# Performance work log

Hardware: AMD Instinct MI355X
Metric: run time of the kernel (lower is better)

## Reference

```python
import jax, jax.numpy as jnp
import numpy as np

N_NODES = 100000
N_EDGES = 1600000
IN_RAW = 64
HID = 128


def setup_inputs() -> dict:
    key = jax.random.key(0)
    ks = jax.random.split(key, 16)
    inp = {
        "x": jax.random.normal(ks[0], (N_NODES, IN_RAW), dtype=jnp.float32),
        "edge_index": jax.random.randint(ks[1], (2, N_EDGES), 0, N_NODES, dtype=jnp.int64),
        "user_ids": jax.random.randint(ks[2], (N_NODES,), 0, 10000, dtype=jnp.int64),
        "locations": jax.random.randint(ks[3], (N_NODES,), 0, 1000, dtype=jnp.int64),
        "time_features": jax.random.normal(ks[4], (N_NODES, 4), dtype=jnp.float32),
        # embeddings / encoders
        "user_emb_table": jax.random.normal(ks[5], (10000, 32), dtype=jnp.float32) * 0.02,
        "loc_emb_table": jax.random.normal(ks[6], (1000, 16), dtype=jnp.float32) * 0.02,
        "W_time": jax.random.normal(ks[7], (4, 16), dtype=jnp.float32) * 0.1,
        "b_time": jnp.zeros((16,), dtype=jnp.float32),
        # SAGEConv 1: lin_l (aggregated, with bias), lin_r (root, no bias)
        "W1_l": jax.random.normal(ks[8], (HID, HID), dtype=jnp.float32) * (1.0 / np.sqrt(HID)),
        "b1": jnp.zeros((HID,), dtype=jnp.float32),
        "W1_r": jax.random.normal(ks[9], (HID, HID), dtype=jnp.float32) * (1.0 / np.sqrt(HID)),
        # SAGEConv 2
        "W2_l": jax.random.normal(ks[10], (HID, HID), dtype=jnp.float32) * (1.0 / np.sqrt(HID)),
        "b2": jnp.zeros((HID,), dtype=jnp.float32),
        "W2_r": jax.random.normal(ks[11], (HID, HID), dtype=jnp.float32) * (1.0 / np.sqrt(HID)),
        # classifier
        "Wc": jax.random.normal(ks[12], (HID, 1), dtype=jnp.float32) * (1.0 / np.sqrt(HID)),
        "bc": jnp.zeros((1,), dtype=jnp.float32),
    }
    return inp


def _sage_conv(h, src, dst, W_l, b_l, W_r, n_nodes):
    # mean aggregation of source features onto targets (PyG SAGEConv default)
    msg_sum = jax.ops.segment_sum(h[src], dst, num_segments=n_nodes)  # [N, D]
    deg = jax.ops.segment_sum(jnp.ones((src.shape[0],), h.dtype), dst, num_segments=n_nodes)
    agg = msg_sum / jnp.maximum(deg, 1.0)[:, None]
    return agg @ W_l + b_l + h @ W_r


def reference(x, edge_index, user_ids, locations, time_features,
              user_emb_table, loc_emb_table, W_time, b_time,
              W1_l, b1, W1_r, W2_l, b2, W2_r, Wc, bc):
    n = x.shape[0]
    src, dst = edge_index[0], edge_index[1]
    user_emb = user_emb_table[user_ids]            # [N, 32]
    loc_emb = loc_emb_table[locations]             # [N, 16]
    time_emb = time_features @ W_time + b_time     # [N, 16]
    h = jnp.concatenate([x, user_emb, loc_emb, time_emb], axis=-1)  # [N, 128]
    h = jax.nn.relu(_sage_conv(h, src, dst, W1_l, b1, W1_r, n))  # dropout = identity (eval)
    h = jax.nn.relu(_sage_conv(h, src, dst, W2_l, b2, W2_r, n))
    return jax.nn.sigmoid(h @ Wc + bc)  # [N, 1]
```

## Files before the change

### kernel.cpp

```cpp
#include <hip/hip_runtime.h>
#include <math.h>

#define N_NODES 100000
#define HID 128
#define NB 782
#define CAP 4096
#define NBLK 256
#define BTILE 6250
#define SUBCAP 32
#define SCAP 3072
#define WPB 64

typedef __attribute__((ext_vector_type(8))) short bf16x8;
typedef __attribute__((ext_vector_type(4))) float f32x4;
typedef __attribute__((ext_vector_type(2))) float f32x2;

__device__ __forceinline__ unsigned short f2bf(float f) {
  union { float f; unsigned u; } v; v.f = f;
  unsigned r = v.u + 0x7FFFu + ((v.u >> 16) & 1u);
  return (unsigned short)(r >> 16);
}
__device__ __forceinline__ unsigned packbf(float lo, float hi) {
  return (unsigned)f2bf(lo) | ((unsigned)f2bf(hi) << 16);
}
__device__ __forceinline__ unsigned pkfp8x4(float a, float b, float c, float d) {
  int v = __builtin_amdgcn_cvt_pk_fp8_f32(a, b, 0, false);
  v = __builtin_amdgcn_cvt_pk_fp8_f32(c, d, v, true);
  return (unsigned)v;
}
__device__ __forceinline__ float bflo(unsigned u) {
  union { unsigned u; float f; } v; v.u = u << 16; return v.f;
}
__device__ __forceinline__ float bfhi(unsigned u) {
  union { unsigned u; float f; } v; v.u = u & 0xFFFF0000u; return v.f;
}
__device__ __forceinline__ void acc_add_fp8(float* a, unsigned w) {
  f32x2 p0 = __builtin_amdgcn_cvt_pk_f32_fp8((int)w, false);
  f32x2 p1 = __builtin_amdgcn_cvt_pk_f32_fp8((int)w, true);
  a[0] += p0.x; a[1] += p0.y; a[2] += p1.x; a[3] += p1.y;
}
__device__ __forceinline__ void acc_add_row(float* a, uint4 u) {
  acc_add_fp8(a + 0, u.x);
  acc_add_fp8(a + 4, u.y);
  acc_add_fp8(a + 8, u.z);
  acc_add_fp8(a + 12, u.w);
}

__global__ __launch_bounds__(256) void k_embed(
    const float* __restrict__ x, const int* __restrict__ uid,
    const int* __restrict__ lid, const float* __restrict__ timef,
    const float* __restrict__ utab, const float* __restrict__ ltab,
    const float* __restrict__ Wt, const float* __restrict__ bt,
    unsigned short* __restrict__ h0, unsigned char* __restrict__ h0f8) {
  int t = threadIdx.x;
  int v = blockIdx.x * 16 + (t >> 4);
  int g = t & 15;
  if (v >= N_NODES) return;
  float val[8];
  if (g < 8) {
    const float4* xp = (const float4*)&x[(size_t)v * 64 + g * 8];
    float4 a = xp[0], b = xp[1];
    val[0] = a.x; val[1] = a.y; val[2] = a.z; val[3] = a.w;
    val[4] = b.x; val[5] = b.y; val[6] = b.z; val[7] = b.w;
  } else if (g < 12) {
    const float4* up = (const float4*)&utab[(size_t)uid[v] * 32 + (g - 8) * 8];
    float4 a = up[0], b = up[1];
    val[0] = a.x; val[1] = a.y; val[2] = a.z; val[3] = a.w;
    val[4] = b.x; val[5] = b.y; val[6] = b.z; val[7] = b.w;
  } else if (g < 14) {
    const float4* lp = (const float4*)&ltab[(size_t)lid[v] * 16 + (g - 12) * 8];
    float4 a = lp[0], b = lp[1];
    val[0] = a.x; val[1] = a.y; val[2] = a.z; val[3] = a.w;
    val[4] = b.x; val[5] = b.y; val[6] = b.z; val[7] = b.w;
  } else {
    int c0 = (g - 14) * 8;
    float4 tf = *(const float4*)&timef[(size_t)v * 4];
#pragma unroll
    for (int i = 0; i < 8; ++i) {
      int c = c0 + i;
      val[i] = bt[c] + tf.x * Wt[c] + tf.y * Wt[16 + c] + tf.z * Wt[32 + c] +
               tf.w * Wt[48 + c];
    }
  }
  uint4 ob;
  ob.x = packbf(val[0], val[1]);
  ob.y = packbf(val[2], val[3]);
  ob.z = packbf(val[4], val[5]);
  ob.w = packbf(val[6], val[7]);
  *(uint4*)&h0[(size_t)v * 128 + g * 8] = ob;
  uint2 of;
  of.x = pkfp8x4(val[0], val[1], val[2], val[3]);
  of.y = pkfp8x4(val[4], val[5], val[6], val[7]);
  *(uint2*)&h0f8[(size_t)v * 128 + g * 8] = of;
}

__global__ __launch_bounds__(512) void k_bucket(
    const int* __restrict__ src, const int* __restrict__ dst,
    int* __restrict__ gcnt, unsigned* __restrict__ bdata2, int E) {
  __shared__ int hcnt[NB];
  int t = threadIdx.x;
  int blk = blockIdx.x;
  int e0 = blk * BTILE;
  int e1 = min(e0 + BTILE, E);
  for (int i = t; i < NB; i += 512) hcnt[i] = 0;
  __syncthreads();
#pragma unroll 4
  for (int e = e0 + t; e < e1; e += 512) {
    int d = dst[e], s = src[e];
    int b = d >> 7;
    int pos = atomicAdd(&hcnt[b], 1);
    if (pos < SUBCAP)
      bdata2[((size_t)blk * NB + b) * SUBCAP + pos] =
          ((unsigned)s << 7) | (unsigned)(d & 127);
  }
  __syncthreads();
  for (int i = t; i < NB; i += 512)
    gcnt[blk * NB + i] = hcnt[i];
}

__global__ __launch_bounds__(256) void k_bfill(
    const int* __restrict__ gcnt, const unsigned* __restrict__ bdata2,
    int* __restrict__ rstart, int* __restrict__ rdeg, int* __restrict__ col,
    const float* __restrict__ W1l, const float* __restrict__ W1r,
    const float* __restrict__ W2l, const float* __restrict__ W2r,
    unsigned short* __restrict__ WT) {
  int b = blockIdx.x;
  int t = threadIdx.x;
  if (b >= NB) {
    int lin = ((b - NB) * 256 + t) * 4;
    int m = lin >> 14;
    int rem = lin & 16383;
    int f = rem >> 7;
    int k0 = rem & 127;
    const float* W = (m == 0) ? W1l : (m == 1) ? W1r : (m == 2) ? W2l : W2r;
    unsigned short o[4];
#pragma unroll
    for (int j = 0; j < 4; ++j) o[j] = f2bf(W[(size_t)(k0 + j) * 128 + f]);
    uint2 pk;
    pk.x = (unsigned)o[0] | ((unsigned)o[1] << 16);
    pk.y = (unsigned)o[2] | ((unsigned)o[3] << 16);
    *(uint2*)&WT[m * 16384 + f * 128 + k0] = pk;
    return;
  }
  __shared__ unsigned sdata[SCAP];
  __shared__ int soff[NBLK];
  __shared__ int scnt[NBLK];
  __shared__ int wsum[4];
  __shared__ int lcnt[128];
  __shared__ int wtot;
  int lane = t & 63, wv = t >> 6;

  int c = (t < NBLK) ? min(gcnt[t * NB + b], SUBCAP) : 0;
  int x = c;
#pragma unroll
  for (int off = 1; off < 64; off <<= 1) {
    int v = __shfl_up(x, off);
    if (lane >= off) x += v;
  }
  if (lane == 63) wsum[wv] = x;
  __syncthreads();
  int add = 0;
#pragma unroll
  for (int k = 0; k < 4; ++k)
    if (k < wv) add += wsum[k];
  x += add;
  int tot = min(wsum[0] + wsum[1] + wsum[2] + wsum[3], SCAP);
  if (t < NBLK) { soff[t] = x - c; scnt[t] = c; }
  if (t < 128) lcnt[t] = 0;
  __syncthreads();

  for (int i = t; i < NBLK * 8; i += 256) {
    int j = i >> 3, p4 = (i & 7) * 4;
    int cj = scnt[j];
    if (p4 < cj) {
      uint4 v = *(const uint4*)&bdata2[((size_t)j * NB + b) * SUBCAP + p4];
      int bs = soff[j] + p4;
      int n = min(4, cj - p4);
      unsigned vv[4] = {v.x, v.y, v.z, v.w};
#pragma unroll
      for (int e = 0; e < 4; ++e)
        if (e < n && bs + e < SCAP) sdata[bs + e] = vv[e];
    }
  }
  __syncthreads();

  for (int i = t; i < tot; i += 256) atomicAdd(&lcnt[sdata[i] & 127u], 1);
  __syncthreads();

  int node0 = b * 128;
  int base = b * CAP;
  if (t < 128) {
    int cc = lcnt[t];
    int xx = cc;
#pragma unroll
    for (int off = 1; off < 64; off <<= 1) {
      int v = __shfl_up(xx, off);
      if (lane >= off) xx += v;
    }
    if (t == 63) wtot = xx;
    __syncthreads();
    if (t >= 64) xx += wtot;
    int excl = xx - cc;
    if (node0 + t < N_NODES) {
      rstart[node0 + t] = base + excl;
      rdeg[node0 + t] = cc;
    }
    lcnt[t] = excl;
  } else {
    __syncthreads();
  }
  __syncthreads();
  for (int i = t; i < tot; i += 256) {
    unsigned v = sdata[i];
    int pos = base + atomicAdd(&lcnt[v & 127u], 1);
    col[pos] = (int)(v >> 7);
  }
}

__global__ __launch_bounds__(256) void k_agg(
    const unsigned char* __restrict__ hf8, const int* __restrict__ rstart,
    const int* __restrict__ rdeg, const int* __restrict__ col,
    unsigned short* __restrict__ agg) {
  int t = threadIdx.x;
  int v = blockIdx.x * 32 + (t >> 3);
  int q = t & 7;
  if (v >= N_NODES) return;
  int s0 = rstart[v];
  int deg = rdeg[v];
  int s1 = s0 + deg;
  const uint4* h8 = (const uint4*)hf8;
  float acc[16];
#pragma unroll
  for (int i = 0; i < 16; ++i) acc[i] = 0.f;
  int j = s0;
  for (; j + 4 <= s1; j += 4) {
    uint4 r0 = h8[(size_t)col[j] * 8 + q];
    uint4 r1 = h8[(size_t)col[j + 1] * 8 + q];
    uint4 r2 = h8[(size_t)col[j + 2] * 8 + q];
    uint4 r3 = h8[(size_t)col[j + 3] * 8 + q];
    acc_add_row(acc, r0);
    acc_add_row(acc, r1);
    acc_add_row(acc, r2);
    acc_add_row(acc, r3);
  }
  for (; j < s1; ++j) acc_add_row(acc, h8[(size_t)col[j] * 8 + q]);
  float inv = 1.f / (float)(deg > 0 ? deg : 1);
  uint4 o0, o1;
  o0.x = packbf(acc[0] * inv, acc[1] * inv);
  o0.y = packbf(acc[2] * inv, acc[3] * inv);
  o0.z = packbf(acc[4] * inv, acc[5] * inv);
  o0.w = packbf(acc[6] * inv, acc[7] * inv);
  o1.x = packbf(acc[8] * inv, acc[9] * inv);
  o1.y = packbf(acc[10] * inv, acc[11] * inv);
  o1.z = packbf(acc[12] * inv, acc[13] * inv);
  o1.w = packbf(acc[14] * inv, acc[15] * inv);
  ((uint4*)agg)[(size_t)v * 16 + q * 2] = o0;
  ((uint4*)agg)[(size_t)v * 16 + q * 2 + 1] = o1;
}

template <bool CLS>
__global__ __launch_bounds__(256, 4) void k_gemm(
    const unsigned short* __restrict__ agg, const unsigned short* __restrict__ hin,
    const unsigned short* __restrict__ WlT, const unsigned short* __restrict__ WrT,
    const float* __restrict__ bias, unsigned short* __restrict__ hout,
    unsigned char* __restrict__ houtf8,
    const float* __restrict__ Wc, const float* __restrict__ bc,
    float* __restrict__ out) {
  __shared__ unsigned short SB[2 * 64 * 136];
  unsigned short* As = SB;
  unsigned short* Hs = SB + 64 * 136;
  unsigned short* Ot = SB;
  float* zred = (float*)SB;
  int t = threadIdx.x;
  int lane = t & 63;
  int wave = t >> 6;
  int wn = wave * 32;
  int l15 = lane & 15;
  int quad = lane >> 4;
  int mbase = blockIdx.x * 64;

  {
    int r = t >> 2, seg = t & 3;
    int gn = mbase + r;
    uint4 av[4], hv[4];
    if (gn < N_NODES) {
      const uint4* ap = (const uint4*)(agg + (size_t)gn * 128 + seg * 32);
      const uint4* hp = (const uint4*)(hin + (size_t)gn * 128 + seg * 32);
#pragma unroll
      for (int i = 0; i < 4; ++i) { av[i] = ap[i]; hv[i] = hp[i]; }
    } else {
#pragma unroll
      for (int i = 0; i < 4; ++i) { av[i] = make_uint4(0,0,0,0); hv[i] = make_uint4(0,0,0,0); }
    }
#pragma unroll
    for (int i = 0; i < 4; ++i) {
      *(uint4*)&As[r * 136 + seg * 32 + i * 8] = av[i];
      *(uint4*)&Hs[r * 136 + seg * 32 + i * 8] = hv[i];
    }
  }
  __syncthreads();

  f32x4 acc4[4][2];
#pragma unroll
  for (int i = 0; i < 4; ++i)
#pragma unroll
    for (int j = 0; j < 2; ++j) acc4[i][j] = (f32x4){0.f, 0.f, 0.f, 0.f};

#pragma unroll
  for (int ks = 0; ks < 4; ++ks) {
    int kb = ks * 32 + quad * 8;
    bf16x8 bL[2], bR[2];
#pragma unroll
    for (int jn = 0; jn < 2; ++jn) {
      int f = wn + jn * 16 + l15;
      bL[jn] = *(const bf16x8*)&WlT[(size_t)f * 128 + kb];
      bR[jn] = *(const bf16x8*)&WrT[(size_t)f * 128 + kb];
    }
    bf16x8 aA[4], aH[4];
#pragma unroll
    for (int im = 0; im < 4; ++im) {
      aA[im] = *(const bf16x8*)&As[(im * 16 + l15) * 136 + kb];
      aH[im] = *(const bf16x8*)&Hs[(im * 16 + l15) * 136 + kb];
    }
#pragma unroll
    for (int im = 0; im < 4; ++im)
#pragma unroll
      for (int jn = 0; jn < 2; ++jn)
        acc4[im][jn] = __builtin_amdgcn_mfma_f32_16x16x32_bf16(
            aA[im], bL[jn], acc4[im][jn], 0, 0, 0);
#pragma unroll
    for (int im = 0; im < 4; ++im)
#pragma unroll
      for (int jn = 0; jn < 2; ++jn)
        acc4[im][jn] = __builtin_amdgcn_mfma_f32_16x16x32_bf16(
            aH[im], bR[jn], acc4[im][jn], 0, 0, 0);
  }

  float bv[2];
#pragma unroll
  for (int jn = 0; jn < 2; ++jn) bv[jn] = bias[wn + jn * 16 + l15];

  __syncthreads();

  if (!CLS) {
#pragma unroll
    for (int im = 0; im < 4; ++im)
#pragma unroll
      for (int rr = 0; rr < 4; ++rr) {
        int rloc = im * 16 + quad * 4 + rr;
#pragma unroll
        for (int jn = 0; jn < 2; ++jn)
          Ot[rloc * 136 + wn + jn * 16 + l15] =
              f2bf(fmaxf(acc4[im][jn][rr] + bv[jn], 0.f));
      }
    __syncthreads();
    int r = t >> 2, seg = t & 3;
    int node = mbase + r;
    if (node < N_NODES) {
      uint4 d0[4];
      const uint4* srcp = (const uint4*)&Ot[r * 136 + seg * 32];
      uint4* dstp = (uint4*)&hout[(size_t)node * 128 + seg * 32];
#pragma unroll
      for (int i = 0; i < 4; ++i) { d0[i] = srcp[i]; dstp[i] = d0[i]; }
      unsigned w[8];
#pragma unroll
      for (int i = 0; i < 4; ++i) {
        unsigned u[4] = {d0[i].x, d0[i].y, d0[i].z, d0[i].w};
#pragma unroll
        for (int p = 0; p < 2; ++p) {
          w[i * 2 + p] = pkfp8x4(bflo(u[p * 2]), bfhi(u[p * 2]),
                                 bflo(u[p * 2 + 1]), bfhi(u[p * 2 + 1]));
        }
      }
      uint4* fp = (uint4*)&houtf8[(size_t)node * 128 + seg * 32];
      fp[0] = make_uint4(w[0], w[1], w[2], w[3]);
      fp[1] = make_uint4(w[4], w[5], w[6], w[7]);
    }
  } else {
    float wcv[2];
#pragma unroll
    for (int jn = 0; jn < 2; ++jn) wcv[jn] = Wc[wn + jn * 16 + l15];
#pragma unroll
    for (int im = 0; im < 4; ++im) {
#pragma unroll
      for (int rr = 0; rr < 4; ++rr) {
        float p = 0.f;
#pragma unroll
        for (int jn = 0; jn < 2; ++jn)
          p += fmaxf(acc4[im][jn][rr] + bv[jn], 0.f) * wcv[jn];
        p += __shfl_xor(p, 1);
        p += __shfl_xor(p, 2);
        p += __shfl_xor(p, 4);
        p += __shfl_xor(p, 8);
        if (l15 == 0) zred[wave * 64 + im * 16 + quad * 4 + rr] = p;
      }
    }
    __syncthreads();
    if (t < 64) {
      int node = mbase + t;
      if (node < N_NODES) {
        float z = zred[t] + zred[64 + t] + zred[128 + t] + zred[192 + t] + bc[0];
        out[node] = 1.f / (1.f + expf(-z));
      }
    }
  }
}

extern "C" void kernel_launch(void* const* d_in, const int* in_sizes, int n_in,
                              void* d_out, int out_size, void* d_ws, size_t ws_size,
                              hipStream_t stream) {
  const float* x     = (const float*)d_in[0];
  const int*   eidx  = (const int*)d_in[1];
  const int*   uid   = (const int*)d_in[2];
  const int*   lid   = (const int*)d_in[3];
  const float* timef = (const float*)d_in[4];
  const float* utab  = (const float*)d_in[5];
  const float* ltab  = (const float*)d_in[6];
  const float* Wt    = (const float*)d_in[7];
  const float* bt    = (const float*)d_in[8];
  const float* W1l   = (const float*)d_in[9];
  const float* b1    = (const float*)d_in[10];
  const float* W1r   = (const float*)d_in[11];
  const float* W2l   = (const float*)d_in[12];
  const float* b2    = (const float*)d_in[13];
  const float* W2r   = (const float*)d_in[14];
  const float* Wc    = (const float*)d_in[15];
  const float* bc    = (const float*)d_in[16];
  float* out = (float*)d_out;

  const int E = in_sizes[1] / 2;
  const int* src = eidx;
  const int* dst = eidx + E;

  char* ws = (char*)d_ws;
  size_t off = 0;
  auto alloc = [&](size_t bytes) -> void* {
    void* p = ws + off;
    off += (bytes + 255) & ~(size_t)255;
    return p;
  };
  const size_t HBYTES = (size_t)N_NODES * 128 * sizeof(unsigned short);
  const size_t FBYTES = (size_t)N_NODES * 128;
  unsigned short* h0  = (unsigned short*)alloc(HBYTES);
  unsigned short* h1  = (unsigned short*)alloc(HBYTES);
  unsigned short* agg = (unsigned short*)alloc(HBYTES);
  unsigned char* h0f8 = (unsigned char*)alloc(FBYTES);
  unsigned char* h1f8 = (unsigned char*)alloc(FBYTES);
  unsigned short* WT  = (unsigned short*)alloc(4 * 16384 * sizeof(unsigned short));
  unsigned* bdata2    = (unsigned*)alloc((size_t)NBLK * NB * SUBCAP * 4);
  int* gcnt           = (int*)alloc((size_t)NBLK * NB * 4);
  int* col            = (int*)alloc((size_t)NB * CAP * 4);
  int* rstart         = (int*)alloc((size_t)N_NODES * 4);
  int* rdeg           = (int*)alloc((size_t)N_NODES * 4);
  (void)ws_size; (void)n_in; (void)out_size;

  k_bucket<<<NBLK, 512, 0, stream>>>(src, dst, gcnt, bdata2, E);
  k_embed<<<(N_NODES + 15) / 16, 256, 0, stream>>>(x, uid, lid, timef, utab, ltab, Wt, bt,
                                                   h0, h0f8);
  k_bfill<<<NB + WPB, 256, 0, stream>>>(gcnt, bdata2, rstart, rdeg, col,
                                        W1l, W1r, W2l, W2r, WT);

  k_agg<<<(N_NODES + 31) / 32, 256, 0, stream>>>(h0f8, rstart, rdeg, col, agg);
  k_gemm<false><<<(N_NODES + 63) / 64, 256, 0, stream>>>(
      agg, h0, WT, WT + 16384, b1, h1, h1f8, nullptr, nullptr, nullptr);

  k_agg<<<(N_NODES + 31) / 32, 256, 0, stream>>>(h1f8, rstart, rdeg, col, agg);
  k_gemm<true><<<(N_NODES + 63) / 64, 256, 0, stream>>>(
      agg, h1, WT + 32768, WT + 49152, b2, nullptr, nullptr, Wc, bc, out);
}
```

Before: 280.1 us.

## Fuse neighbor aggregation into the per-layer GEMM kernel, dropping agg buffer

Merges the gather-mean aggregation and the dual GEMM into one k_layer kernel. Each block aggregates its 64 nodes straight into shared memory, and the root features are read directly from global memory into MFMA operands instead of being staged in LDS. This removes a global write and re-read of the bf16 agg array and one launch per layer, and halves LDS use so occupancy can rise (launch bounds raised to 5). The cost is that the gather latency and the GEMM now share one block, with fewer nodes per block during the gather phase (64 nodes over two passes), and the uncoalesced global loads of hin inside the MFMA loop.

Result: no change. 285.3 us (+1.9%).

```diff
diff --git a/kernel.cpp b/kernel.cpp
--- a/kernel.cpp
+++ b/kernel.cpp
@@ -217,88 +217,71 @@
   }
 }
 
-__global__ __launch_bounds__(256) void k_agg(
-    const unsigned char* __restrict__ hf8, const int* __restrict__ rstart,
-    const int* __restrict__ rdeg, const int* __restrict__ col,
-    unsigned short* __restrict__ agg) {
-  int t = threadIdx.x;
-  int v = blockIdx.x * 32 + (t >> 3);
-  int q = t & 7;
-  if (v >= N_NODES) return;
-  int s0 = rstart[v];
-  int deg = rdeg[v];
-  int s1 = s0 + deg;
-  const uint4* h8 = (const uint4*)hf8;
-  float acc[16];
-#pragma unroll
-  for (int i = 0; i < 16; ++i) acc[i] = 0.f;
-  int j = s0;
-  for (; j + 4 <= s1; j += 4) {
-    uint4 r0 = h8[(size_t)col[j] * 8 + q];
-    uint4 r1 = h8[(size_t)col[j + 1] * 8 + q];
-    uint4 r2 = h8[(size_t)col[j + 2] * 8 + q];
-    uint4 r3 = h8[(size_t)col[j + 3] * 8 + q];
-    acc_add_row(acc, r0);
-    acc_add_row(acc, r1);
-    acc_add_row(acc, r2);
-    acc_add_row(acc, r3);
-  }
-  for (; j < s1; ++j) acc_add_row(acc, h8[(size_t)col[j] * 8 + q]);
-  float inv = 1.f / (float)(deg > 0 ? deg : 1);
-  uint4 o0, o1;
-  o0.x = packbf(acc[0] * inv, acc[1] * inv);
-  o0.y = packbf(acc[2] * inv, acc[3] * inv);
-  o0.z = packbf(acc[4] * inv, acc[5] * inv);
-  o0.w = packbf(acc[6] * inv, acc[7] * inv);
-  o1.x = packbf(acc[8] * inv, acc[9] * inv);
-  o1.y = packbf(acc[10] * inv, acc[11] * inv);
-  o1.z = packbf(acc[12] * inv, acc[13] * inv);
-  o1.w = packbf(acc[14] * inv, acc[15] * inv);
-  ((uint4*)agg)[(size_t)v * 16 + q * 2] = o0;
-  ((uint4*)agg)[(size_t)v * 16 + q * 2 + 1] = o1;
-}
-
 template <bool CLS>
-__global__ __launch_bounds__(256, 4) void k_gemm(
-    const unsigned short* __restrict__ agg, const unsigned short* __restrict__ hin,
+__global__ __launch_bounds__(256, 5) void k_layer(
+    const unsigned char* __restrict__ hf8, const unsigned short* __restrict__ hin,
+    const int* __restrict__ rstart, const int* __restrict__ rdeg,
+    const int* __restrict__ col,
     const unsigned short* __restrict__ WlT, const unsigned short* __restrict__ WrT,
     const float* __restrict__ bias, unsigned short* __restrict__ hout,
     unsigned char* __restrict__ houtf8,
     const float* __restrict__ Wc, const float* __restrict__ bc,
     float* __restrict__ out) {
-  __shared__ unsigned short SB[2 * 64 * 136];
-  unsigned short* As = SB;
-  unsigned short* Hs = SB + 64 * 136;
-  unsigned short* Ot = SB;
-  float* zred = (float*)SB;
+  __shared__ unsigned short As[64 * 136];
+  unsigned short* Ot = As;
+  float* zred = (float*)As;
   int t = threadIdx.x;
+  int mbase = blockIdx.x * 64;
+
+  {
+    int q = t & 7;
+    const uint4* h8 = (const uint4*)hf8;
+#pragma unroll
+    for (int pass = 0; pass < 2; ++pass) {
+      int ln = pass * 32 + (t >> 3);
+      int v = mbase + ln;
+      float acc[16];
+#pragma unroll
+      for (int i = 0; i < 16; ++i) acc[i] = 0.f;
+      int deg = 0;
+      if (v < N_NODES) {
+        int s0 = rstart[v];
+        deg = rdeg[v];
+        int s1 = s0 + deg;
+        int j = s0;
+        for (; j + 4 <= s1; j += 4) {
+          uint4 r0 = h8[(size_t)col[j] * 8 + q];
+          uint4 r1 = h8[(size_t)col[j + 1] * 8 + q];
+          uint4 r2 = h8[(size_t)col[j + 2] * 8 + q];
+          uint4 r3 = h8[(size_t)col[j + 3] * 8 + q];
+          acc_add_row(acc, r0);
+          acc_add_row(acc, r1);
+          acc_add_row(acc, r2);
+          acc_add_row(acc, r3);
+        }
+        for (; j < s1; ++j) acc_add_row(acc, h8[(size_t)col[j] * 8 + q]);
+      }
+      float inv = 1.f / (float)(deg > 0 ? deg : 1);
+      uint4 o0, o1;
+      o0.x = packbf(acc[0] * inv, acc[1] * inv);
+      o0.y = packbf(acc[2] * inv, acc[3] * inv);
+      o0.z = packbf(acc[4] * inv, acc[5] * inv);
+      o0.w = packbf(acc[6] * inv, acc[7] * inv);
+      o1.x = packbf(acc[8] * inv, acc[9] * inv);
+      o1.y = packbf(acc[10] * inv, acc[11] * inv);
+      o1.z = packbf(acc[12] * inv, acc[13] * inv);
+      o1.w = packbf(acc[14] * inv, acc[15] * inv);
+      *(uint4*)&As[ln * 136 + q * 16] = o0;
+      *(uint4*)&As[ln * 136 + q * 16 + 8] = o1;
+    }
+  }
+  __syncthreads();
+
   int lane = t & 63;
   int wave = t >> 6;
   int wn = wave * 32;
   int l15 = lane & 15;
   int quad = lane >> 4;
-  int mbase = blockIdx.x * 64;
-
-  {
-    int r = t >> 2, seg = t & 3;
-    int gn = mbase + r;
-    uint4 av[4], hv[4];
-    if (gn < N_NODES) {
-      const uint4* ap = (const uint4*)(agg + (size_t)gn * 128 + seg * 32);
-      const uint4* hp = (const uint4*)(hin + (size_t)gn * 128 + seg * 32);
-#pragma unroll
-      for (int i = 0; i < 4; ++i) { av[i] = ap[i]; hv[i] = hp[i]; }
-    } else {
-#pragma unroll
-      for (int i = 0; i < 4; ++i) { av[i] = make_uint4(0,0,0,0); hv[i] = make_uint4(0,0,0,0); }
-    }
-#pragma unroll
-    for (int i = 0; i < 4; ++i) {
-      *(uint4*)&As[r * 136 + seg * 32 + i * 8] = av[i];
-      *(uint4*)&Hs[r * 136 + seg * 32 + i * 8] = hv[i];
-    }
-  }
-  __syncthreads();
 
   f32x4 acc4[4][2];
 #pragma unroll
@@ -306,6 +289,7 @@
 #pragma unroll
     for (int j = 0; j < 2; ++j) acc4[i][j] = (f32x4){0.f, 0.f, 0.f, 0.f};
 
+  const bf16x8 zf = {0, 0, 0, 0, 0, 0, 0, 0};
 #pragma unroll
   for (int ks = 0; ks < 4; ++ks) {
     int kb = ks * 32 + quad * 8;
@@ -319,8 +303,9 @@
     bf16x8 aA[4], aH[4];
 #pragma unroll
     for (int im = 0; im < 4; ++im) {
+      int node = mbase + im * 16 + l15;
       aA[im] = *(const bf16x8*)&As[(im * 16 + l15) * 136 + kb];
-      aH[im] = *(const bf16x8*)&Hs[(im * 16 + l15) * 136 + kb];
+      aH[im] = (node < N_NODES) ? *(const bf16x8*)&hin[(size_t)node * 128 + kb] : zf;
     }
 #pragma unroll
     for (int im = 0; im < 4; ++im)
@@ -443,7 +428,6 @@
   const size_t FBYTES = (size_t)N_NODES * 128;
   unsigned short* h0  = (unsigned short*)alloc(HBYTES);
   unsigned short* h1  = (unsigned short*)alloc(HBYTES);
-  unsigned short* agg = (unsigned short*)alloc(HBYTES);
   unsigned char* h0f8 = (unsigned char*)alloc(FBYTES);
   unsigned char* h1f8 = (unsigned char*)alloc(FBYTES);
   unsigned short* WT  = (unsigned short*)alloc(4 * 16384 * sizeof(unsigned short));
@@ -460,11 +444,11 @@
   k_bfill<<<NB + WPB, 256, 0, stream>>>(gcnt, bdata2, rstart, rdeg, col,
                                         W1l, W1r, W2l, W2r, WT);
 
-  k_agg<<<(N_NODES + 31) / 32, 256, 0, stream>>>(h0f8, rstart, rdeg, col, agg);
-  k_gemm<false><<<(N_NODES + 63) / 64, 256, 0, stream>>>(
-      agg, h0, WT, WT + 16384, b1, h1, h1f8, nullptr, nullptr, nullptr);
-
-  k_agg<<<(N_NODES + 31) / 32, 256, 0, stream>>>(h1f8, rstart, rdeg, col, agg);
-  k_gemm<true><<<(N_NODES + 63) / 64, 256, 0, stream>>>(
-      agg, h1, WT + 32768, WT + 49152, b2, nullptr, nullptr, Wc, bc, out);
-}
+  k_layer<false><<<(N_NODES + 63) / 64, 256, 0, stream>>>(
+      h0f8, h0, rstart, rdeg, col, WT, WT + 16384, b1, h1, h1f8,
+      nullptr, nullptr, nullptr);
+
+  k_layer<true><<<(N_NODES + 63) / 64, 256, 0, stream>>>(
+      h1f8, h1, rstart, rdeg, col, WT + 32768, WT + 49152, b2, nullptr, nullptr,
+      Wc, bc, out);
+}
```
